# Optimization experiments

Hardware: AMD Instinct MI355X
Metric: run time of the kernel (lower is better)

Reference implementation:

```python
import jax, jax.numpy as jnp
from jax import lax
import numpy as np

T_DATA, E_NO, I_NO, SUB_NO, T_SYN = 100000, 1000, 1000, 20, 201

def setup_inputs() -> dict:
    key = jax.random.key(0)
    ks = jax.random.split(key, 10)
    return {
        'S_e': jax.random.uniform(ks[0], (T_DATA, E_NO), jnp.float32),
        'S_i': jax.random.uniform(ks[1], (T_DATA, I_NO), jnp.float32),
        'C_syn_e': jax.random.uniform(ks[2], (SUB_NO, E_NO), jnp.float32),
        'C_syn_i': jax.random.uniform(ks[3], (SUB_NO, I_NO), jnp.float32),
        'C_den': jax.random.uniform(ks[4], (SUB_NO, SUB_NO), jnp.float32),
        'w_e': jax.random.normal(ks[5], (SUB_NO, T_SYN), jnp.float32),
        'b_e': jax.random.normal(ks[6], (SUB_NO,), jnp.float32),
        'w_i': jax.random.normal(ks[7], (SUB_NO, T_SYN), jnp.float32),
        'b_i': jax.random.normal(ks[8], (SUB_NO,), jnp.float32),
        'W_s_s_sub': jax.random.uniform(ks[9], (SUB_NO,), jnp.float32),
    }

def _depthwise_causal_conv(x_ts, w, b, T_syn):
    # x_ts: [T, sub]; torch pads T_syn-1 zeros at the front then runs
    # grouped Conv1d (cross-correlation) with VALID padding -> length T.
    T, sub = x_ts.shape
    pad = jnp.zeros((T_syn - 1, sub), x_ts.dtype)
    xin = jnp.concatenate([pad, x_ts], axis=0).T[None]          # [1, sub, T+T_syn-1]
    out = lax.conv_general_dilated(xin, w[:, None, :], (1,), 'VALID',
                                   feature_group_count=sub,
                                   dimension_numbers=('NCH', 'OIH', 'NCH'))
    return out[0].T + b                                          # [T, sub]

def reference(S_e, S_i, C_syn_e, C_syn_i, C_den, w_e, b_e, w_i, b_i, W_s_s_sub):
    T_syn = w_e.shape[1]
    syn_e = S_e @ C_syn_e.T                                      # [T, sub]
    syn_i = S_i @ C_syn_i.T                                      # [T, sub]
    syn_e_in = _depthwise_causal_conv(syn_e, w_e, b_e, T_syn)
    syn_i_in = _depthwise_causal_conv(syn_i, w_i, b_i, T_syn)
    syn_in = syn_e_in + syn_i_in                                 # [T, sub]
    # one hop of dendritic-tree message passing: child -> parent via C_den
    Y_s_pad = syn_in + (syn_in * jnp.exp(W_s_s_sub)) @ C_den.T   # [T, sub]
    final_voltage = Y_s_pad[:, 0] * jnp.exp(W_s_s_sub[0])        # [T]
    return (final_voltage, Y_s_pad, Y_s_pad)
```

## Files before the change

kernel.cpp:

```cpp
#include <hip/hip_runtime.h>

#define T_DATA 100000
#define E_NO   1000
#define SUB    20
#define TSYN   201
#define PITCH  521

__global__ __launch_bounds__(256) void k1_matmul(
    const float* __restrict__ S_e, const float* __restrict__ S_i,
    const float* __restrict__ C_e, const float* __restrict__ C_i,
    float* __restrict__ sy_e, float* __restrict__ sy_i)
{
    const int lane = threadIdx.x & 63;
    const int q = __builtin_amdgcn_readfirstlane(threadIdx.x >> 6);
    const int row = blockIdx.x * 64 + lane;
    const float* __restrict__ Sp = blockIdx.y ? S_i : S_e;
    const float* __restrict__ Cp = blockIdx.y ? C_i : C_e;
    float* __restrict__ outp = blockIdx.y ? sy_i : sy_e;

    float acc[SUB];
#pragma unroll
    for (int s = 0; s < SUB; ++s) acc[s] = 0.f;

    if (row < T_DATA) {
        const float* rp = Sp + (size_t)row * E_NO;
        for (int j = q; j < 250; j += 4) {
            const float4 sv = *reinterpret_cast<const float4*>(rp + 4 * j);
#pragma unroll
            for (int s = 0; s < SUB; ++s) {
                const float4 c4 = *reinterpret_cast<const float4*>(Cp + s * E_NO + 4 * j);
                acc[s] = fmaf(sv.x, c4.x, acc[s]);
                acc[s] = fmaf(sv.y, c4.y, acc[s]);
                acc[s] = fmaf(sv.z, c4.z, acc[s]);
                acc[s] = fmaf(sv.w, c4.w, acc[s]);
            }
        }
    }

    __shared__ float red[3 * 64 * 21];
    if (q > 0) {
#pragma unroll
        for (int s = 0; s < SUB; ++s) red[((q - 1) * 64 + lane) * 21 + s] = acc[s];
    }
    __syncthreads();
    if (q == 0 && row < T_DATA) {
#pragma unroll
        for (int p = 0; p < 3; ++p)
#pragma unroll
            for (int s = 0; s < SUB; ++s) acc[s] += red[(p * 64 + lane) * 21 + s];
        float* op = outp + (size_t)row * SUB;
#pragma unroll
        for (int c = 0; c < 5; ++c) {
            float4 v = make_float4(acc[4 * c], acc[4 * c + 1], acc[4 * c + 2], acc[4 * c + 3]);
            *reinterpret_cast<float4*>(op + 4 * c) = v;
        }
    }
}

__global__ __launch_bounds__(320) void k2_conv_epi(
    const float* __restrict__ sy_e, const float* __restrict__ sy_i,
    const float* __restrict__ w_e, const float* __restrict__ b_e,
    const float* __restrict__ w_i, const float* __restrict__ b_i,
    const float* __restrict__ Cden, const float* __restrict__ Wss,
    float* __restrict__ dout)
{
    __shared__ float A0[SUB * PITCH];
    __shared__ float A1[SUB * PITCH];
    const int tid = threadIdx.x;
    const int tb  = blockIdx.x * 256;

    for (int m = 0; m < 15; ++m) {
        int idx = tid + 320 * m;
        if (idx >= 4560) break;
        int a   = idx >= 2280;
        int id2 = idx - a * 2280;
        int u   = id2 / 5;
        int c   = id2 - 5 * u;
        int t   = tb - 200 + u;
        float4 v = make_float4(0.f, 0.f, 0.f, 0.f);
        const float* src = a ? sy_i : sy_e;
        if (t >= 0 && t < T_DATA) v = *reinterpret_cast<const float4*>(src + t * SUB + 4 * c);
        float* dst = a ? A1 : A0;
        const int sw = u + (u >> 3);
        dst[(4 * c + 0) * PITCH + sw] = v.x;
        dst[(4 * c + 1) * PITCH + sw] = v.y;
        dst[(4 * c + 2) * PITCH + sw] = v.z;
        dst[(4 * c + 3) * PITCH + sw] = v.w;
    }
    __syncthreads();

    const int lane = tid & 63;
    const int g    = tid >> 6;
    const int t_l  = lane & 15;
    const int s_l  = lane >> 4;
    const int s    = 4 * g + s_l;

    float out[16];
    const float bias = b_e[s] + b_i[s];
#pragma unroll
    for (int i = 0; i < 16; ++i) out[i] = bias;

    const int rb = s * PITCH + 18 * t_l;

#pragma unroll 1
    for (int cv = 0; cv < 2; ++cv) {
        const float* Ap = cv ? A1 : A0;
        const float* wp = (cv ? w_i : w_e) + s * TSYN;
        float W0[16], W1[16];
#pragma unroll
        for (int j = 0; j < 16; ++j) W0[j] = Ap[rb + j + (j >> 3)];
#pragma unroll
        for (int j = 0; j < 16; ++j) W1[j] = Ap[rb + 16 + j + ((16 + j) >> 3)];
#pragma unroll 1
        for (int c = 0; c < 12; ++c) {
            float wreg[16];
#pragma unroll
            for (int kk = 0; kk < 16; ++kk) wreg[kk] = wp[16 * c + kk];
#pragma unroll
            for (int kk = 0; kk < 16; ++kk) {
                const float wv = wreg[kk];
#pragma unroll
                for (int i = 0; i < 16; ++i) {
                    const int ix = kk + i;
                    const float av = (ix < 16) ? W0[ix] : W1[ix - 16];
                    out[i] = fmaf(wv, av, out[i]);
                }
            }
#pragma unroll
            for (int j = 0; j < 16; ++j) W0[j] = W1[j];
            const int co = 16 * c + 32;
            const int cb = rb + co + (co >> 3);
#pragma unroll
            for (int j = 0; j < 16; ++j) W1[j] = Ap[cb + j + (j >> 3)];
        }
        {
            float wreg[9];
#pragma unroll
            for (int kk = 0; kk < 9; ++kk) wreg[kk] = wp[192 + kk];
#pragma unroll
            for (int kk = 0; kk < 9; ++kk) {
                const float wv = wreg[kk];
#pragma unroll
                for (int i = 0; i < 16; ++i) {
                    const int ix = kk + i;
                    const float av = (ix < 16) ? W0[ix] : W1[ix - 16];
                    out[i] = fmaf(wv, av, out[i]);
                }
            }
        }
    }

    __syncthreads();
    float* Yt = A0;
#pragma unroll
    for (int i = 0; i < 16; ++i) Yt[(16 * t_l + i) * 21 + s] = out[i];
    __syncthreads();

    if (tid < 256) {
        const int t = tb + tid;
        if (t < T_DATA) {
            float* __restrict__ volt = dout;
            float* __restrict__ Y1 = dout + T_DATA;
            float* __restrict__ Y2 = dout + T_DATA + (size_t)T_DATA * SUB;
            float row[SUB], uu[SUB];
#pragma unroll
            for (int sp = 0; sp < SUB; ++sp) {
                const float r = Yt[tid * 21 + sp];
                row[sp] = r;
                uu[sp]  = r * expf(Wss[sp]);
            }
            float y[SUB];
#pragma unroll
            for (int s2 = 0; s2 < SUB; ++s2) {
                float a2 = row[s2];
#pragma unroll
                for (int sp = 0; sp < SUB; ++sp)
                    a2 = fmaf(Cden[s2 * SUB + sp], uu[sp], a2);
                y[s2] = a2;
            }
            float* o1 = Y1 + (size_t)t * SUB;
            float* o2 = Y2 + (size_t)t * SUB;
#pragma unroll
            for (int c = 0; c < 5; ++c) {
                float4 v = make_float4(y[4 * c], y[4 * c + 1], y[4 * c + 2], y[4 * c + 3]);
                *reinterpret_cast<float4*>(o1 + 4 * c) = v;
                *reinterpret_cast<float4*>(o2 + 4 * c) = v;
            }
            volt[t] = y[0] * expf(Wss[0]);
        }
    }
}

extern "C" void kernel_launch(void* const* d_in, const int* in_sizes, int n_in,
                              void* d_out, int out_size, void* d_ws, size_t ws_size,
                              hipStream_t stream)
{
    const float* S_e  = (const float*)d_in[0];
    const float* S_i  = (const float*)d_in[1];
    const float* C_e  = (const float*)d_in[2];
    const float* C_i  = (const float*)d_in[3];
    const float* Cden = (const float*)d_in[4];
    const float* w_e  = (const float*)d_in[5];
    const float* b_e  = (const float*)d_in[6];
    const float* w_i  = (const float*)d_in[7];
    const float* b_i  = (const float*)d_in[8];
    const float* Wss  = (const float*)d_in[9];
    float* out  = (float*)d_out;
    float* sy_e = (float*)d_ws;
    float* sy_i = sy_e + (size_t)T_DATA * SUB;

    dim3 g1(1563, 2);
    k1_matmul<<<g1, 256, 0, stream>>>(S_e, S_i, C_e, C_i, sy_e, sy_i);
    k2_conv_epi<<<391, 320, 0, stream>>>(sy_e, sy_i, w_e, b_e, w_i, b_i,
                                         Cden, Wss, out);
}
```

Baseline: 982.5 us.

## Stage transposed weights in LDS, two rows per lane, halve conv tile

```diff
diff --git a/kernel.cpp b/kernel.cpp
--- a/kernel.cpp
+++ b/kernel.cpp
@@ -4,58 +4,110 @@
 #define E_NO   1000
 #define SUB    20
 #define TSYN   201
-#define PITCH  521
 
 __global__ __launch_bounds__(256) void k1_matmul(
     const float* __restrict__ S_e, const float* __restrict__ S_i,
     const float* __restrict__ C_e, const float* __restrict__ C_i,
     float* __restrict__ sy_e, float* __restrict__ sy_i)
 {
-    const int lane = threadIdx.x & 63;
-    const int q = __builtin_amdgcn_readfirstlane(threadIdx.x >> 6);
-    const int row = blockIdx.x * 64 + lane;
+    __shared__ float4 CT[250 * SUB];
+    const int tid = threadIdx.x;
     const float* __restrict__ Sp = blockIdx.y ? S_i : S_e;
     const float* __restrict__ Cp = blockIdx.y ? C_i : C_e;
     float* __restrict__ outp = blockIdx.y ? sy_i : sy_e;
 
-    float acc[SUB];
-#pragma unroll
-    for (int s = 0; s < SUB; ++s) acc[s] = 0.f;
-
-    if (row < T_DATA) {
-        const float* rp = Sp + (size_t)row * E_NO;
-        for (int j = q; j < 250; j += 4) {
-            const float4 sv = *reinterpret_cast<const float4*>(rp + 4 * j);
+    {
+        const float4* __restrict__ C4 = reinterpret_cast<const float4*>(Cp);
+        for (int i = tid; i < 250 * SUB; i += 256) {
+            const int s = i / 250, j = i - s * 250;
+            CT[j * SUB + s] = C4[i];
+        }
+    }
+    __syncthreads();
+
+    const int lane  = tid & 63;
+    const int wv    = tid >> 6;
+    const int strip = blockIdx.x * 4 + wv;
+    const int r0 = strip * 128 + lane;
+    const int r1 = r0 + 64;
+    const int cr0 = r0 < T_DATA ? r0 : T_DATA - 1;
+    const int cr1 = r1 < T_DATA ? r1 : T_DATA - 1;
+
+    const float4* __restrict__ p0 = reinterpret_cast<const float4*>(Sp + (size_t)cr0 * E_NO);
+    const float4* __restrict__ p1 = reinterpret_cast<const float4*>(Sp + (size_t)cr1 * E_NO);
+
+    float acc0[SUB], acc1[SUB];
+#pragma unroll
+    for (int s = 0; s < SUB; ++s) { acc0[s] = 0.f; acc1[s] = 0.f; }
+
+    float4 ca[4], cb[4];
+#pragma unroll
+    for (int k = 0; k < 4; ++k) { ca[k] = p0[k]; cb[k] = p1[k]; }
+
+    for (int jb = 0; jb < 62; ++jb) {
+        float4 na[4], nb[4];
+        const int nbase = 4 * jb + 4;
+#pragma unroll
+        for (int k = 0; k < 4; ++k) {
+            const int idx = (nbase + k < 250) ? nbase + k : 249;
+            na[k] = p0[idx]; nb[k] = p1[idx];
+        }
+#pragma unroll
+        for (int k = 0; k < 4; ++k) {
+            const float4* __restrict__ crow = &CT[(4 * jb + k) * SUB];
+            const float4 av = ca[k], bv = cb[k];
 #pragma unroll
             for (int s = 0; s < SUB; ++s) {
-                const float4 c4 = *reinterpret_cast<const float4*>(Cp + s * E_NO + 4 * j);
-                acc[s] = fmaf(sv.x, c4.x, acc[s]);
-                acc[s] = fmaf(sv.y, c4.y, acc[s]);
-                acc[s] = fmaf(sv.z, c4.z, acc[s]);
-                acc[s] = fmaf(sv.w, c4.w, acc[s]);
-            }
-        }
-    }
-
-    __shared__ float red[3 * 64 * 21];
-    if (q > 0) {
-#pragma unroll
-        for (int s = 0; s < SUB; ++s) red[((q - 1) * 64 + lane) * 21 + s] = acc[s];
-    }
-    __syncthreads();
-    if (q == 0 && row < T_DATA) {
-#pragma unroll
-        for (int p = 0; p < 3; ++p)
-#pragma unroll
-            for (int s = 0; s < SUB; ++s) acc[s] += red[(p * 64 + lane) * 21 + s];
-        float* op = outp + (size_t)row * SUB;
-#pragma unroll
-        for (int c = 0; c < 5; ++c) {
-            float4 v = make_float4(acc[4 * c], acc[4 * c + 1], acc[4 * c + 2], acc[4 * c + 3]);
-            *reinterpret_cast<float4*>(op + 4 * c) = v;
-        }
+                const float4 c4 = crow[s];
+                acc0[s] = fmaf(av.x, c4.x, acc0[s]);
+                acc0[s] = fmaf(av.y, c4.y, acc0[s]);
+                acc0[s] = fmaf(av.z, c4.z, acc0[s]);
+                acc0[s] = fmaf(av.w, c4.w, acc0[s]);
+                acc1[s] = fmaf(bv.x, c4.x, acc1[s]);
+                acc1[s] = fmaf(bv.y, c4.y, acc1[s]);
+                acc1[s] = fmaf(bv.z, c4.z, acc1[s]);
+                acc1[s] = fmaf(bv.w, c4.w, acc1[s]);
+            }
+        }
+#pragma unroll
+        for (int k = 0; k < 4; ++k) { ca[k] = na[k]; cb[k] = nb[k]; }
+    }
+#pragma unroll
+    for (int k = 0; k < 2; ++k) {
+        const float4* __restrict__ crow = &CT[(248 + k) * SUB];
+        const float4 av = ca[k], bv = cb[k];
+#pragma unroll
+        for (int s = 0; s < SUB; ++s) {
+            const float4 c4 = crow[s];
+            acc0[s] = fmaf(av.x, c4.x, acc0[s]);
+            acc0[s] = fmaf(av.y, c4.y, acc0[s]);
+            acc0[s] = fmaf(av.z, c4.z, acc0[s]);
+            acc0[s] = fmaf(av.w, c4.w, acc0[s]);
+            acc1[s] = fmaf(bv.x, c4.x, acc1[s]);
+            acc1[s] = fmaf(bv.y, c4.y, acc1[s]);
+            acc1[s] = fmaf(bv.z, c4.z, acc1[s]);
+            acc1[s] = fmaf(bv.w, c4.w, acc1[s]);
+        }
+    }
+
+    if (r0 < T_DATA) {
+        float* op = outp + (size_t)r0 * SUB;
+#pragma unroll
+        for (int c = 0; c < 5; ++c)
+            *reinterpret_cast<float4*>(op + 4 * c) =
+                make_float4(acc0[4*c], acc0[4*c+1], acc0[4*c+2], acc0[4*c+3]);
+    }
+    if (r1 < T_DATA) {
+        float* op = outp + (size_t)r1 * SUB;
+#pragma unroll
+        for (int c = 0; c < 5; ++c)
+            *reinterpret_cast<float4*>(op + 4 * c) =
+                make_float4(acc1[4*c], acc1[4*c+1], acc1[4*c+2], acc1[4*c+3]);
     }
 }
+
+#define KROWS 328
+#define P2    369
 
 __global__ __launch_bounds__(320) void k2_conv_epi(
     const float* __restrict__ sy_e, const float* __restrict__ sy_i,
@@ -64,16 +116,16 @@
     const float* __restrict__ Cden, const float* __restrict__ Wss,
     float* __restrict__ dout)
 {
-    __shared__ float A0[SUB * PITCH];
-    __shared__ float A1[SUB * PITCH];
+    __shared__ float A0[SUB * P2];
+    __shared__ float A1[SUB * P2];
     const int tid = threadIdx.x;
-    const int tb  = blockIdx.x * 256;
-
-    for (int m = 0; m < 15; ++m) {
+    const int tb  = blockIdx.x * 128;
+
+    for (int m = 0; m < 11; ++m) {
         int idx = tid + 320 * m;
-        if (idx >= 4560) break;
-        int a   = idx >= 2280;
-        int id2 = idx - a * 2280;
+        if (idx >= 3280) break;
+        int a   = idx >= 1640;
+        int id2 = idx - a * 1640;
         int u   = id2 / 5;
         int c   = id2 - 5 * u;
         int t   = tb - 200 + u;
@@ -82,10 +134,10 @@
         if (t >= 0 && t < T_DATA) v = *reinterpret_cast<const float4*>(src + t * SUB + 4 * c);
         float* dst = a ? A1 : A0;
         const int sw = u + (u >> 3);
-        dst[(4 * c + 0) * PITCH + sw] = v.x;
-        dst[(4 * c + 1) * PITCH + sw] = v.y;
-        dst[(4 * c + 2) * PITCH + sw] = v.z;
-        dst[(4 * c + 3) * PITCH + sw] = v.w;
+        dst[(4 * c + 0) * P2 + sw] = v.x;
+        dst[(4 * c + 1) * P2 + sw] = v.y;
+        dst[(4 * c + 2) * P2 + sw] = v.z;
+        dst[(4 * c + 3) * P2 + sw] = v.w;
     }
     __syncthreads();
 
@@ -95,68 +147,60 @@
     const int s_l  = lane >> 4;
     const int s    = 4 * g + s_l;
 
-    float out[16];
+    float out[8];
     const float bias = b_e[s] + b_i[s];
 #pragma unroll
-    for (int i = 0; i < 16; ++i) out[i] = bias;
-
-    const int rb = s * PITCH + 18 * t_l;
+    for (int i = 0; i < 8; ++i) out[i] = bias;
+
+    const int rb = s * P2 + 9 * t_l;
 
 #pragma unroll 1
     for (int cv = 0; cv < 2; ++cv) {
         const float* Ap = cv ? A1 : A0;
         const float* wp = (cv ? w_i : w_e) + s * TSYN;
-        float W0[16], W1[16];
-#pragma unroll
-        for (int j = 0; j < 16; ++j) W0[j] = Ap[rb + j + (j >> 3)];
-#pragma unroll
-        for (int j = 0; j < 16; ++j) W1[j] = Ap[rb + 16 + j + ((16 + j) >> 3)];
+        float W0[8], W1[8];
+#pragma unroll
+        for (int j = 0; j < 8; ++j) W0[j] = Ap[rb + j];
+#pragma unroll
+        for (int j = 0; j < 8; ++j) W1[j] = Ap[rb + 9 + j];
 #pragma unroll 1
-        for (int c = 0; c < 12; ++c) {
-            float wreg[16];
-#pragma unroll
-            for (int kk = 0; kk < 16; ++kk) wreg[kk] = wp[16 * c + kk];
-#pragma unroll
-            for (int kk = 0; kk < 16; ++kk) {
-                const float wv = wreg[kk];
-#pragma unroll
-                for (int i = 0; i < 16; ++i) {
+        for (int c = 0; c < 25; ++c) {
+            float wr[8];
+#pragma unroll
+            for (int kk = 0; kk < 8; ++kk) wr[kk] = wp[8 * c + kk];
+#pragma unroll
+            for (int kk = 0; kk < 8; ++kk) {
+                const float wv = wr[kk];
+#pragma unroll
+                for (int i = 0; i < 8; ++i) {
                     const int ix = kk + i;
-                    const float av = (ix < 16) ? W0[ix] : W1[ix - 16];
+                    const float av = (ix < 8) ? W0[ix] : W1[ix - 8];
                     out[i] = fmaf(wv, av, out[i]);
                 }
             }
 #pragma unroll
-            for (int j = 0; j < 16; ++j) W0[j] = W1[j];
-            const int co = 16 * c + 32;
-            const int cb = rb + co + (co >> 3);
-#pragma unroll
-            for (int j = 0; j < 16; ++j) W1[j] = Ap[cb + j + (j >> 3)];
+            for (int j = 0; j < 8; ++j) W0[j] = W1[j];
+            if (c < 24) {
+                const int co = 8 * c + 16;
+                const int cb = rb + co + (co >> 3);
+#pragma unroll
+                for (int j = 0; j < 8; ++j) W1[j] = Ap[cb + j];
+            }
         }
         {
-            float wreg[9];
-#pragma unroll
-            for (int kk = 0; kk < 9; ++kk) wreg[kk] = wp[192 + kk];
-#pragma unroll
-            for (int kk = 0; kk < 9; ++kk) {
-                const float wv = wreg[kk];
-#pragma unroll
-                for (int i = 0; i < 16; ++i) {
-                    const int ix = kk + i;
-                    const float av = (ix < 16) ? W0[ix] : W1[ix - 16];
-                    out[i] = fmaf(wv, av, out[i]);
-                }
-            }
+            const float wlast = wp[200];
+#pragma unroll
+            for (int i = 0; i < 8; ++i) out[i] = fmaf(wlast, W0[i], out[i]);
         }
     }
 
     __syncthreads();
     float* Yt = A0;
 #pragma unroll
-    for (int i = 0; i < 16; ++i) Yt[(16 * t_l + i) * 21 + s] = out[i];
-    __syncthreads();
-
-    if (tid < 256) {
+    for (int i = 0; i < 8; ++i) Yt[(8 * t_l + i) * 21 + s] = out[i];
+    __syncthreads();
+
+    if (tid < 128) {
         const int t = tb + tid;
         if (t < T_DATA) {
             float* __restrict__ volt = dout;
@@ -182,7 +226,7 @@
             float* o2 = Y2 + (size_t)t * SUB;
 #pragma unroll
             for (int c = 0; c < 5; ++c) {
-                float4 v = make_float4(y[4 * c], y[4 * c + 1], y[4 * c + 2], y[4 * c + 3]);
+                float4 v = make_float4(y[4*c], y[4*c+1], y[4*c+2], y[4*c+3]);
                 *reinterpret_cast<float4*>(o1 + 4 * c) = v;
                 *reinterpret_cast<float4*>(o2 + 4 * c) = v;
             }
@@ -209,8 +253,8 @@
     float* sy_e = (float*)d_ws;
     float* sy_i = sy_e + (size_t)T_DATA * SUB;
 
-    dim3 g1(1563, 2);
+    dim3 g1(196, 2);
     k1_matmul<<<g1, 256, 0, stream>>>(S_e, S_i, C_e, C_i, sy_e, sy_i);
-    k2_conv_epi<<<391, 320, 0, stream>>>(sy_e, sy_i, w_e, b_e, w_i, b_i,
+    k2_conv_epi<<<782, 320, 0, stream>>>(sy_e, sy_i, w_e, b_e, w_i, b_i,
                                          Cden, Wss, out);
 }
```

After: 995.0 us. No clear change (+1.3%).
